# Kernel tuning notes

Measured on AMD Instinct MI355X. Metric: run time of the kernel, lower is better.

## Reference

```python
import jax, jax.numpy as jnp
import numpy as np

HIDDEN = 1024
ATT = 512

def _xavier(key, shape):
    fan_in, fan_out = shape[0], shape[1]
    bound = float(np.sqrt(6.0 / (fan_in + fan_out)))
    return jax.random.uniform(key, shape, jnp.float32, -bound, bound)

def setup_inputs() -> dict:
    key = jax.random.key(0)
    ks = jax.random.split(key, 7)
    B, P = 256, 196
    spatial_image = jax.random.normal(ks[0], (B, P, HIDDEN), jnp.float32)
    decoder_out = jax.random.normal(ks[1], (B, HIDDEN), jnp.float32)
    st = jax.random.normal(ks[2], (B, HIDDEN), jnp.float32)
    # weights stored as (in_dim, out_dim); math identical to torch Linear(x @ W.T)
    W_cnn = _xavier(ks[3], (HIDDEN, ATT))
    W_dec = _xavier(ks[4], (HIDDEN, ATT))
    W_sen = _xavier(ks[5], (HIDDEN, ATT))
    W_att = _xavier(ks[6], (ATT, 1))
    return {"spatial_image": spatial_image, "decoder_out": decoder_out, "st": st,
            "W_cnn": W_cnn, "W_dec": W_dec, "W_sen": W_sen, "W_att": W_att}

def reference(spatial_image, decoder_out, st, W_cnn, W_dec, W_sen, W_att):
    # dropout in eval mode (identity)
    cnn_out = jnp.einsum('bph,ha->bpa', spatial_image, W_cnn)   # (B,P,A)
    dec_out = decoder_out @ W_dec                                # (B,A)
    addition = jnp.tanh(cnn_out + dec_out[:, None, :])           # (B,P,A)
    zt = jnp.einsum('bpa,a->bp', addition, W_att[:, 0])          # (B,P)
    alpha_t = jax.nn.softmax(zt, axis=1)                         # (B,P)
    ct = jnp.einsum('bph,bp->bh', spatial_image, alpha_t)        # (B,H)
    sen = jnp.tanh(dec_out + st @ W_sen)                         # (B,A)
    out = sen @ W_att                                            # (B,1)
    concat = jnp.concatenate([zt, out], axis=1)                  # (B,P+1)
    alpha_hat = jax.nn.softmax(concat, axis=1)
    beta_t = alpha_hat[:, -1:]                                   # (B,1)
    c_hat = beta_t * st + (1.0 - beta_t) * ct                    # (B,H)
    return (alpha_t, beta_t, c_hat)
```

## Files before the change

kernel.cpp:

```cpp
#include <hip/hip_runtime.h>
#include <hip/hip_bf16.h>

#define BATCH   256
#define NP      196
#define HIDDEN  1024
#define ATT     512
#define M_TOTAL (BATCH * NP)
#define BM 128
#define BN 256
#define BK 32
#define MT_TILES (M_TOTAL / BM)
#define NB_TILES (ATT / BN)

typedef __attribute__((ext_vector_type(8))) short bf16x8v;
typedef __attribute__((ext_vector_type(4))) float f32x4;

__device__ inline unsigned short f2bf(float x) {
    unsigned int u = __float_as_uint(x);
    u += 0x7fffu + ((u >> 16) & 1u);
    return (unsigned short)(u >> 16);
}

__device__ __forceinline__ unsigned int pk2bf(float lo, float hi) {
    unsigned int r;
    asm("v_cvt_pk_bf16_f32 %0, %1, %2" : "=v"(r) : "v"(lo), "v"(hi));
    return r;
}

__device__ inline float fast_tanh(float x) {
    float e = __expf(2.0f * x);
    return 1.0f - 2.0f / (e + 1.0f);
}

__device__ __forceinline__ void glds16(const void* gsrc, void* ldst) {
    __builtin_amdgcn_global_load_lds(
        (const __attribute__((address_space(1))) unsigned int*)gsrc,
        (__attribute__((address_space(3))) unsigned int*)ldst,
        16, 0, 0);
}

__global__ void k0_arrange(const float* __restrict__ Wc, unsigned short* __restrict__ Wt) {
    int g = blockIdx.x * 256 + threadIdx.x;
    int nb    = g >> 15;
    int rem   = g & 32767;
    int kt    = rem >> 10;
    int chunk = (rem >> 8) & 3;
    int n     = rem & 255;
    int col   = nb * 256 + n;
    int kb    = kt * 32 + chunk * 8;
    unsigned short v[8];
#pragma unroll
    for (int j = 0; j < 8; ++j) v[j] = f2bf(Wc[(size_t)(kb + j) * ATT + col]);
    uint4 pk;
    pk.x = (unsigned int)v[0] | ((unsigned int)v[1] << 16);
    pk.y = (unsigned int)v[2] | ((unsigned int)v[3] << 16);
    pk.z = (unsigned int)v[4] | ((unsigned int)v[5] << 16);
    pk.w = (unsigned int)v[6] | ((unsigned int)v[7] << 16);
    *(uint4*)(Wt + (size_t)g * 8) = pk;
}

__global__ void k1_small(const float* __restrict__ dec_in, const float* __restrict__ st,
                         const float* __restrict__ Wdec,  const float* __restrict__ Wsen,
                         float* __restrict__ dec_out, float* __restrict__ stw) {
    const float* X = blockIdx.z ? st   : dec_in;
    const float* W = blockIdx.z ? Wsen : Wdec;
    float*       O = blockIdx.z ? stw  : dec_out;
    int ci = threadIdx.x & 31;
    int c0 = blockIdx.x * 128 + ci * 4;
    int b  = blockIdx.y * 8 + (threadIdx.x >> 5);
    const float* x = X + (size_t)b * HIDDEN;
    float4 acc = {0.f, 0.f, 0.f, 0.f};
    for (int k = 0; k < HIDDEN; k += 4) {
#pragma unroll
        for (int kk = 0; kk < 4; ++kk) {
            float4 w = *(const float4*)(W + (size_t)(k + kk) * ATT + c0);
            float a = x[k + kk];
            acc.x += a * w.x; acc.y += a * w.y; acc.z += a * w.z; acc.w += a * w.w;
        }
    }
    *(float4*)(O + (size_t)b * ATT + c0) = acc;
}

__global__ void __launch_bounds__(512, 4)
k2_fused_gemm(const float* __restrict__ A, const unsigned short* __restrict__ Wt,
              const float* __restrict__ dec, const float* __restrict__ Watt,
              float* __restrict__ ztp) {
    __shared__ __align__(16) unsigned short Abuf[4 * 128 * 8];
    __shared__ __align__(16) unsigned short Bbuf[4 * 256 * 8];
    __shared__ float zred[128 * 4];

    const int tid = threadIdx.x;
    const int w  = tid >> 6;
    const int l  = tid & 63;
    const int lg = l >> 4, ll = l & 15;
    const int wr = w >> 2, wc = w & 3;

    const int bid = (int)blockIdx.x;
    const int swz = (bid & 7) * 98 + (bid >> 3);
    const int mt = swz >> 1, nb = swz & 1;
    const int r0 = mt * BM;
    const int c0 = nb * BN;

    f32x4 acc[4][4];
#pragma unroll
    for (int m = 0; m < 4; ++m)
#pragma unroll
        for (int n = 0; n < 4; ++n) acc[m][n] = (f32x4){0.f, 0.f, 0.f, 0.f};

    const int arow = tid >> 2;
    const int ach  = tid & 3;
    const float* aptr = A + (size_t)(r0 + arow) * HIDDEN + ach * 8;
    unsigned short* aslot = Abuf + (ach * 128 + arow) * 8;

    const size_t wt_base = (size_t)nb * 32 * 8192;
    const char* bsrc0 = (const char*)(Wt + wt_base) + (w * 2 + 0) * 1024 + l * 16;
    const char* bsrc1 = (const char*)(Wt + wt_base) + (w * 2 + 1) * 1024 + l * 16;
    char* bdst0 = (char*)Bbuf + (w * 2 + 0) * 1024 + l * 16;
    char* bdst1 = (char*)Bbuf + (w * 2 + 1) * 1024 + l * 16;

    float4 a0 = *(const float4*)(aptr);
    float4 a1 = *(const float4*)(aptr + 4);

    for (int kt = 0; kt < 32; ++kt) {
        __syncthreads();

        glds16(bsrc0 + kt * 16384, bdst0);
        glds16(bsrc1 + kt * 16384, bdst1);

        uint4 ap;
        ap.x = pk2bf(a0.x, a0.y);
        ap.y = pk2bf(a0.z, a0.w);
        ap.z = pk2bf(a1.x, a1.y);
        ap.w = pk2bf(a1.z, a1.w);
        *(uint4*)aslot = ap;

        __syncthreads();

        if (kt < 31) {
            a0 = *(const float4*)(aptr + (kt + 1) * 32);
            a1 = *(const float4*)(aptr + (kt + 1) * 32 + 4);
        }

        bf16x8v af[4], bfr[4];
#pragma unroll
        for (int m = 0; m < 4; ++m)
            af[m] = *(const bf16x8v*)(Abuf + ((lg * 128 + wr * 64 + m * 16 + ll) << 3));
#pragma unroll
        for (int n = 0; n < 4; ++n)
            bfr[n] = *(const bf16x8v*)(Bbuf + ((lg * 256 + wc * 64 + n * 16 + ll) << 3));
#pragma unroll
        for (int m = 0; m < 4; ++m)
#pragma unroll
            for (int n = 0; n < 4; ++n)
                acc[m][n] = __builtin_amdgcn_mfma_f32_16x16x32_bf16(af[m], bfr[n], acc[m][n], 0, 0, 0);
    }

    const int clocal = wc * 64 + ll;
    float watt[4];
#pragma unroll
    for (int n = 0; n < 4; ++n) watt[n] = Watt[c0 + clocal + n * 16];

#pragma unroll
    for (int m = 0; m < 4; ++m) {
#pragma unroll
        for (int j = 0; j < 4; ++j) {
            int rl = wr * 64 + m * 16 + lg * 4 + j;
            int rowg = r0 + rl;
            int b = rowg / NP;
            const float* db = dec + (size_t)b * ATT + c0;
            float s = 0.f;
#pragma unroll
            for (int n = 0; n < 4; ++n)
                s += fast_tanh(acc[m][n][j] + db[clocal + n * 16]) * watt[n];
            s += __shfl_xor(s, 1);
            s += __shfl_xor(s, 2);
            s += __shfl_xor(s, 4);
            s += __shfl_xor(s, 8);
            if (ll == 0) zred[rl * 4 + wc] = s;
        }
    }
    __syncthreads();
    if (tid < 128) {
        float t = zred[tid * 4] + zred[tid * 4 + 1] + zred[tid * 4 + 2] + zred[tid * 4 + 3];
        ztp[(size_t)nb * M_TOTAL + r0 + tid] = t;
    }
}

__global__ void k3_softmax(const float* __restrict__ dec, const float* __restrict__ stw,
                           const float* __restrict__ Watt, const float* __restrict__ ztp,
                           float* __restrict__ out, float* __restrict__ beta_ws) {
    int b = blockIdx.x;
    int t = threadIdx.x;
    __shared__ float red[256];

    float p = 0.f;
#pragma unroll
    for (int c = t; c < ATT; c += 256)
        p += fast_tanh(dec[(size_t)b * ATT + c] + stw[(size_t)b * ATT + c]) * Watt[c];
    red[t] = p;
    __syncthreads();
    for (int s = 128; s > 0; s >>= 1) { if (t < s) red[t] += red[t + s]; __syncthreads(); }
    float outv = red[0];
    __syncthreads();

    float z = -1e30f;
    if (t < NP) z = ztp[b * NP + t] + ztp[M_TOTAL + b * NP + t];
    red[t] = z;
    __syncthreads();
    for (int s = 128; s > 0; s >>= 1) { if (t < s) red[t] = fmaxf(red[t], red[t + s]); __syncthreads(); }
    float m1 = red[0];
    __syncthreads();

    float e = (t < NP) ? __expf(z - m1) : 0.f;
    red[t] = e;
    __syncthreads();
    for (int s = 128; s > 0; s >>= 1) { if (t < s) red[t] += red[t + s]; __syncthreads(); }
    float s1 = red[0];

    if (t < NP) out[b * NP + t] = e / s1;

    if (t == 0) {
        float m2 = fmaxf(m1, outv);
        float s2 = s1 * __expf(m1 - m2) + __expf(outv - m2);
        float beta = __expf(outv - m2) / s2;
        out[M_TOTAL + b] = beta;
        beta_ws[b] = beta;
    }
}

__global__ void k4_ct(const float* __restrict__ spatial, const float* __restrict__ alpha,
                      float* __restrict__ ctp) {
    int q = blockIdx.x;
    int b = blockIdx.y;
    int t = threadIdx.x;
    __shared__ float al[49];
    if (t < 49) al[t] = alpha[b * NP + q * 49 + t];
    __syncthreads();
    const float* sp = spatial + (size_t)b * NP * HIDDEN + (size_t)q * 49 * HIDDEN + t * 4;
    float4 acc = {0.f, 0.f, 0.f, 0.f};
#pragma unroll 7
    for (int p = 0; p < 49; ++p) {
        float4 v = *(const float4*)(sp + (size_t)p * HIDDEN);
        float a = al[p];
        acc.x += a * v.x; acc.y += a * v.y; acc.z += a * v.z; acc.w += a * v.w;
    }
    *(float4*)(ctp + ((size_t)q * BATCH + b) * HIDDEN + t * 4) = acc;
}

__global__ void k5_chat(const float* __restrict__ st, const float* __restrict__ ctp,
                        const float* __restrict__ beta, float* __restrict__ chat) {
    int g = blockIdx.x * 256 + threadIdx.x;
    int b = g >> 8;
    int h0 = (g & 255) * 4;
    float be = beta[b];
    float4 s = *(const float4*)(st + (size_t)b * HIDDEN + h0);
    float4 c = {0.f, 0.f, 0.f, 0.f};
#pragma unroll
    for (int q = 0; q < 4; ++q) {
        float4 v = *(const float4*)(ctp + ((size_t)q * BATCH + b) * HIDDEN + h0);
        c.x += v.x; c.y += v.y; c.z += v.z; c.w += v.w;
    }
    float4 o;
    o.x = be * s.x + (1.f - be) * c.x;
    o.y = be * s.y + (1.f - be) * c.y;
    o.z = be * s.z + (1.f - be) * c.z;
    o.w = be * s.w + (1.f - be) * c.w;
    *(float4*)(chat + (size_t)b * HIDDEN + h0) = o;
}

extern "C" void kernel_launch(void* const* d_in, const int* in_sizes, int n_in,
                              void* d_out, int out_size, void* d_ws, size_t ws_size,
                              hipStream_t stream) {
    const float* spatial = (const float*)d_in[0];
    const float* decoder = (const float*)d_in[1];
    const float* st      = (const float*)d_in[2];
    const float* Wcnn    = (const float*)d_in[3];
    const float* Wdec    = (const float*)d_in[4];
    const float* Wsen    = (const float*)d_in[5];
    const float* Watt    = (const float*)d_in[6];
    float* out = (float*)d_out;

    char* ws = (char*)d_ws;
    unsigned short* Wt = (unsigned short*)(ws + 0);
    float* ztp  = (float*)(ws + 1048576);
    float* dec  = (float*)(ws + 1449984);
    float* stw  = (float*)(ws + 1974272);
    float* beta = (float*)(ws + 2498560);
    float* ctp  = (float*)(ws + 2499584);

    k0_arrange<<<256, 256, 0, stream>>>(Wcnn, Wt);
    k1_small<<<dim3(4, 32, 2), 256, 0, stream>>>(decoder, st, Wdec, Wsen, dec, stw);
    k2_fused_gemm<<<MT_TILES * NB_TILES, 512, 0, stream>>>(spatial, Wt, dec, Watt, ztp);
    k3_softmax<<<256, 256, 0, stream>>>(dec, stw, Watt, ztp, out, beta);
    k4_ct<<<dim3(4, 256), 256, 0, stream>>>(spatial, out, ctp);
    k5_chat<<<256, 256, 0, stream>>>(st, ctp, beta, out + M_TOTAL + BATCH);
}
```

Baseline: 186.2 us.

## Retile fused GEMM to 256x128x64 with double-buffered swizzled LDS pipeline

Restructures the main cnn GEMM kernel: the tile becomes 256x128 with BK=64, and LDS is double-buffered so the global loads of the next A/B tile overlap MFMA work on the current one. An XOR swizzle is applied to both the weight pre-arrangement and the A staging layout to avoid LDS bank conflicts, and MFMA sections run under raised priority. Since N is now split into 4 tiles, four partial zt sums are written and summed in the softmax kernel, and workspace offsets grow. The larger LDS footprint and register use lower occupancy to one block per CU.

```diff
diff --git a/kernel.cpp b/kernel.cpp
--- a/kernel.cpp
+++ b/kernel.cpp
@@ -6,11 +6,12 @@
 #define HIDDEN  1024
 #define ATT     512
 #define M_TOTAL (BATCH * NP)
-#define BM 128
-#define BN 256
-#define BK 32
+#define BM 256
+#define BN 128
+#define BK 64
+#define NB_TILES (ATT / BN)
 #define MT_TILES (M_TOTAL / BM)
-#define NB_TILES (ATT / BN)
+#define KTILES   (HIDDEN / BK)
 
 typedef __attribute__((ext_vector_type(8))) short bf16x8v;
 typedef __attribute__((ext_vector_type(4))) float f32x4;
@@ -41,16 +42,16 @@
 
 __global__ void k0_arrange(const float* __restrict__ Wc, unsigned short* __restrict__ Wt) {
     int g = blockIdx.x * 256 + threadIdx.x;
-    int nb    = g >> 15;
-    int rem   = g & 32767;
-    int kt    = rem >> 10;
-    int chunk = (rem >> 8) & 3;
-    int n     = rem & 255;
-    int col   = nb * 256 + n;
-    int kb    = kt * 32 + chunk * 8;
+    int nb  = g >> 14;
+    int kt  = (g >> 10) & 15;
+    int col = (g >> 3) & 127;
+    int cp  = g & 7;
+    int c   = cp ^ (col & 7);
+    int kb  = kt * 64 + c * 8;
+    int colg = nb * 128 + col;
     unsigned short v[8];
 #pragma unroll
-    for (int j = 0; j < 8; ++j) v[j] = f2bf(Wc[(size_t)(kb + j) * ATT + col]);
+    for (int j = 0; j < 8; ++j) v[j] = f2bf(Wc[(size_t)(kb + j) * ATT + colg]);
     uint4 pk;
     pk.x = (unsigned int)v[0] | ((unsigned int)v[1] << 16);
     pk.y = (unsigned int)v[2] | ((unsigned int)v[3] << 16);
@@ -81,13 +82,13 @@
     *(float4*)(O + (size_t)b * ATT + c0) = acc;
 }
 
-__global__ void __launch_bounds__(512, 4)
+__global__ void __launch_bounds__(512, 1)
 k2_fused_gemm(const float* __restrict__ A, const unsigned short* __restrict__ Wt,
               const float* __restrict__ dec, const float* __restrict__ Watt,
               float* __restrict__ ztp) {
-    __shared__ __align__(16) unsigned short Abuf[4 * 128 * 8];
-    __shared__ __align__(16) unsigned short Bbuf[4 * 256 * 8];
-    __shared__ float zred[128 * 4];
+    __shared__ __align__(16) char ldsA[2][32768];
+    __shared__ __align__(16) char ldsB[2][16384];
+    __shared__ float zred[1024];
 
     const int tid = threadIdx.x;
     const int w  = tid >> 6;
@@ -97,80 +98,142 @@
 
     const int bid = (int)blockIdx.x;
     const int swz = (bid & 7) * 98 + (bid >> 3);
-    const int mt = swz >> 1, nb = swz & 1;
+    const int mt = swz >> 2, nb = swz & 3;
     const int r0 = mt * BM;
     const int c0 = nb * BN;
 
-    f32x4 acc[4][4];
-#pragma unroll
-    for (int m = 0; m < 4; ++m)
-#pragma unroll
-        for (int n = 0; n < 4; ++n) acc[m][n] = (f32x4){0.f, 0.f, 0.f, 0.f};
-
-    const int arow = tid >> 2;
-    const int ach  = tid & 3;
-    const float* aptr = A + (size_t)(r0 + arow) * HIDDEN + ach * 8;
-    unsigned short* aslot = Abuf + (ach * 128 + arow) * 8;
-
-    const size_t wt_base = (size_t)nb * 32 * 8192;
-    const char* bsrc0 = (const char*)(Wt + wt_base) + (w * 2 + 0) * 1024 + l * 16;
-    const char* bsrc1 = (const char*)(Wt + wt_base) + (w * 2 + 1) * 1024 + l * 16;
-    char* bdst0 = (char*)Bbuf + (w * 2 + 0) * 1024 + l * 16;
-    char* bdst1 = (char*)Bbuf + (w * 2 + 1) * 1024 + l * 16;
-
-    float4 a0 = *(const float4*)(aptr);
-    float4 a1 = *(const float4*)(aptr + 4);
-
-    for (int kt = 0; kt < 32; ++kt) {
-        __syncthreads();
-
-        glds16(bsrc0 + kt * 16384, bdst0);
-        glds16(bsrc1 + kt * 16384, bdst1);
-
-        uint4 ap;
-        ap.x = pk2bf(a0.x, a0.y);
-        ap.y = pk2bf(a0.z, a0.w);
-        ap.z = pk2bf(a1.x, a1.y);
-        ap.w = pk2bf(a1.z, a1.w);
-        *(uint4*)aslot = ap;
-
-        __syncthreads();
-
-        if (kt < 31) {
-            a0 = *(const float4*)(aptr + (kt + 1) * 32);
-            a1 = *(const float4*)(aptr + (kt + 1) * 32 + 4);
+    f32x4 acc[8][2];
+#pragma unroll
+    for (int m = 0; m < 8; ++m)
+#pragma unroll
+        for (int n = 0; n < 2; ++n) acc[m][n] = (f32x4){0.f, 0.f, 0.f, 0.f};
+
+    const float* asrc = A + (size_t)(r0 + (tid >> 4)) * HIDDEN + (tid & 15) * 4;
+    const int aw_off = ((tid >> 4) * 128)
+                     + (((((tid >> 1) & 7) ^ ((tid >> 4) & 7))) << 4)
+                     + ((tid & 1) << 3);
+    const char* bimg = (const char*)Wt + (size_t)nb * (KTILES * 16384);
+
+#define AF_READS(Ab, kk)                                                        \
+    _Pragma("unroll")                                                           \
+    for (int m = 0; m < 8; ++m)                                                 \
+        af[m] = *(const bf16x8v*)((Ab) + (wr * 128 + m * 16 + ll) * 128 +       \
+                                  ((((kk) * 4 + lg) ^ (ll & 7)) << 4));
+#define BF_READS(Bb, kk)                                                        \
+    _Pragma("unroll")                                                           \
+    for (int n = 0; n < 2; ++n)                                                 \
+        bfr[n] = *(const bf16x8v*)((Bb) + (wc * 32 + n * 16 + ll) * 128 +       \
+                                   ((((kk) * 4 + lg) ^ (ll & 7)) << 4));
+#define MFMA16                                                                  \
+    _Pragma("unroll")                                                           \
+    for (int m = 0; m < 8; ++m)                                                 \
+        _Pragma("unroll")                                                       \
+        for (int n = 0; n < 2; ++n)                                             \
+            acc[m][n] = __builtin_amdgcn_mfma_f32_16x16x32_bf16(                \
+                af[m], bfr[n], acc[m][n], 0, 0, 0);
+#define LGKM0_FENCE do {                                                        \
+    asm volatile("s_waitcnt lgkmcnt(0)" ::: "memory");                          \
+    __builtin_amdgcn_sched_barrier(0);                                          \
+} while (0)
+#define BAR __builtin_amdgcn_s_barrier()
+
+    char* Acur = ldsA[0]; char* Anxt = ldsA[1];
+    char* Bcur = ldsB[0]; char* Bnxt = ldsB[1];
+    float4 av[8];
+
+#pragma unroll
+    for (int j = 0; j < 8; ++j)
+        av[j] = *(const float4*)(asrc + (size_t)j * 32 * HIDDEN);
+    glds16(bimg + 0    + tid * 16, Bcur + 0    + tid * 16);
+    glds16(bimg + 8192 + tid * 16, Bcur + 8192 + tid * 16);
+#pragma unroll
+    for (int j = 0; j < 8; ++j) {
+        uint2 u;
+        u.x = pk2bf(av[j].x, av[j].y);
+        u.y = pk2bf(av[j].z, av[j].w);
+        *(uint2*)(Acur + j * 4096 + aw_off) = u;
+    }
+    asm volatile("s_waitcnt vmcnt(0)" ::: "memory");
+    LGKM0_FENCE;
+    BAR;
+
+    for (int t = 0; t < 15; ++t) {
+        {
+            bf16x8v af[8], bfr[2];
+            AF_READS(Acur, 0); BF_READS(Bcur, 0);
+#pragma unroll
+            for (int j = 0; j < 8; ++j)
+                av[j] = *(const float4*)(asrc + (size_t)j * 32 * HIDDEN + (t + 1) * 64);
+            glds16(bimg + (size_t)(t + 1) * 16384 + 0    + tid * 16, Bnxt + 0    + tid * 16);
+            glds16(bimg + (size_t)(t + 1) * 16384 + 8192 + tid * 16, Bnxt + 8192 + tid * 16);
+            BAR;
+            LGKM0_FENCE;
+            __builtin_amdgcn_s_setprio(1);
+            MFMA16;
+            __builtin_amdgcn_s_setprio(0);
+            BAR;
         }
-
-        bf16x8v af[4], bfr[4];
-#pragma unroll
-        for (int m = 0; m < 4; ++m)
-            af[m] = *(const bf16x8v*)(Abuf + ((lg * 128 + wr * 64 + m * 16 + ll) << 3));
-#pragma unroll
-        for (int n = 0; n < 4; ++n)
-            bfr[n] = *(const bf16x8v*)(Bbuf + ((lg * 256 + wc * 64 + n * 16 + ll) << 3));
-#pragma unroll
-        for (int m = 0; m < 4; ++m)
-#pragma unroll
-            for (int n = 0; n < 4; ++n)
-                acc[m][n] = __builtin_amdgcn_mfma_f32_16x16x32_bf16(af[m], bfr[n], acc[m][n], 0, 0, 0);
-    }
-
-    const int clocal = wc * 64 + ll;
-    float watt[4];
-#pragma unroll
-    for (int n = 0; n < 4; ++n) watt[n] = Watt[c0 + clocal + n * 16];
-
-#pragma unroll
-    for (int m = 0; m < 4; ++m) {
+        {
+            bf16x8v af[8], bfr[2];
+            AF_READS(Acur, 1); BF_READS(Bcur, 1);
+#pragma unroll
+            for (int j = 0; j < 8; ++j) {
+                uint2 u;
+                u.x = pk2bf(av[j].x, av[j].y);
+                u.y = pk2bf(av[j].z, av[j].w);
+                *(uint2*)(Anxt + j * 4096 + aw_off) = u;
+            }
+            BAR;
+            LGKM0_FENCE;
+            __builtin_amdgcn_s_setprio(1);
+            MFMA16;
+            __builtin_amdgcn_s_setprio(0);
+            asm volatile("s_waitcnt vmcnt(0)" ::: "memory");
+            BAR;
+        }
+        char* tA = Acur; Acur = Anxt; Anxt = tA;
+        char* tB = Bcur; Bcur = Bnxt; Bnxt = tB;
+    }
+
+    {
+        bf16x8v af[8], bfr[2];
+        AF_READS(Acur, 0); BF_READS(Bcur, 0);
+        LGKM0_FENCE;
+        __builtin_amdgcn_s_setprio(1);
+        MFMA16;
+        __builtin_amdgcn_s_setprio(0);
+    }
+    {
+        bf16x8v af[8], bfr[2];
+        AF_READS(Acur, 1); BF_READS(Bcur, 1);
+        LGKM0_FENCE;
+        __builtin_amdgcn_s_setprio(1);
+        MFMA16;
+        __builtin_amdgcn_s_setprio(0);
+    }
+
+#undef AF_READS
+#undef BF_READS
+#undef MFMA16
+#undef LGKM0_FENCE
+#undef BAR
+
+    const int clocal = wc * 32 + ll;
+    float watt[2];
+#pragma unroll
+    for (int n = 0; n < 2; ++n) watt[n] = Watt[c0 + clocal + n * 16];
+
+#pragma unroll
+    for (int m = 0; m < 8; ++m) {
 #pragma unroll
         for (int j = 0; j < 4; ++j) {
-            int rl = wr * 64 + m * 16 + lg * 4 + j;
+            int rl = wr * 128 + m * 16 + lg * 4 + j;
             int rowg = r0 + rl;
             int b = rowg / NP;
             const float* db = dec + (size_t)b * ATT + c0;
             float s = 0.f;
 #pragma unroll
-            for (int n = 0; n < 4; ++n)
+            for (int n = 0; n < 2; ++n)
                 s += fast_tanh(acc[m][n][j] + db[clocal + n * 16]) * watt[n];
             s += __shfl_xor(s, 1);
             s += __shfl_xor(s, 2);
@@ -180,7 +243,7 @@
         }
     }
     __syncthreads();
-    if (tid < 128) {
+    if (tid < 256) {
         float t = zred[tid * 4] + zred[tid * 4 + 1] + zred[tid * 4 + 2] + zred[tid * 4 + 3];
         ztp[(size_t)nb * M_TOTAL + r0 + tid] = t;
     }
@@ -204,7 +267,10 @@
     __syncthreads();
 
     float z = -1e30f;
-    if (t < NP) z = ztp[b * NP + t] + ztp[M_TOTAL + b * NP + t];
+    if (t < NP) {
+        z = ztp[b * NP + t] + ztp[M_TOTAL + b * NP + t]
+          + ztp[2 * M_TOTAL + b * NP + t] + ztp[3 * M_TOTAL + b * NP + t];
+    }
     red[t] = z;
     __syncthreads();
     for (int s = 128; s > 0; s >>= 1) { if (t < s) red[t] = fmaxf(red[t], red[t + s]); __syncthreads(); }
@@ -283,10 +349,10 @@
     char* ws = (char*)d_ws;
     unsigned short* Wt = (unsigned short*)(ws + 0);
     float* ztp  = (float*)(ws + 1048576);
-    float* dec  = (float*)(ws + 1449984);
-    float* stw  = (float*)(ws + 1974272);
-    float* beta = (float*)(ws + 2498560);
-    float* ctp  = (float*)(ws + 2499584);
+    float* dec  = (float*)(ws + 1851392);
+    float* stw  = (float*)(ws + 2375680);
+    float* beta = (float*)(ws + 2899968);
+    float* ctp  = (float*)(ws + 2901504);
 
     k0_arrange<<<256, 256, 0, stream>>>(Wcnn, Wt);
     k1_small<<<dim3(4, 32, 2), 256, 0, stream>>>(decoder, st, Wdec, Wsen, dec, stw);
```

Result: slower. 232.4 us (+24.8%).
